# Kernel tuning notes

Measured on AMD Instinct MI355X. Metric: run time of the kernel, lower is better.

The kernel has to match this reference:

```python
import jax, jax.numpy as jnp
import numpy as np

LABEL_SIZE = 64
START = LABEL_SIZE - 2
STOP = LABEL_SIZE - 1
NEG = -10000.0


def setup_inputs() -> dict:
    key = jax.random.key(0)
    k1, k2 = jax.random.split(key)
    B, T, L = 512, 512, LABEL_SIZE
    emissions = jax.random.normal(k1, (B, T, L), dtype=jnp.float32)
    # xavier-uniform-ish init, then mask row START (nothing transitions INTO start
    # ... actually transitions[next, prev]: row START = transitions into START)
    bound = float(np.sqrt(6.0 / (L + L)))
    trans = jax.random.uniform(k2, (L, L), dtype=jnp.float32, minval=-bound, maxval=bound)
    trans = trans.at[START, :].set(NEG)   # never transition to START
    trans = trans.at[:, STOP].set(NEG)    # never transition from STOP
    return {"input": emissions, "transitions": trans}


def reference(input, transitions):
    # input: [B, T, L] emission scores; transitions[next_tag, prev_tag]: [L, L]
    B, T, L = input.shape
    init = jnp.full((B, L), NEG, dtype=input.dtype).at[:, START].set(0.0)

    def step(forward_var, emit_t):
        # forward_var: [B, L] (over prev tag); emit_t: [B, L] (over next tag)
        # scores[b, next, prev] = forward_var[b, prev] + transitions[next, prev]
        nv = jax.nn.logsumexp(forward_var[:, None, :] + transitions[None, :, :], axis=-1)
        return nv + emit_t, None

    forward_var, _ = jax.lax.scan(step, init, jnp.swapaxes(input, 0, 1))  # scan over T
    terminal = forward_var + transitions[STOP][None, :]
    return jax.nn.logsumexp(terminal, axis=-1)  # [B] log partition function
```

## Files before the change

### kernel.cpp

```cpp
#include <hip/hip_runtime.h>

#define NTAG 64
#define TLEN 512
#define START_TAG 62
#define STOP_TAG 63
#define NB 16

typedef __attribute__((ext_vector_type(4))) float    f32x4;
typedef __attribute__((ext_vector_type(8))) short    s16x8;
typedef __attribute__((ext_vector_type(2))) unsigned u32x2;
typedef __attribute__((ext_vector_type(4))) unsigned u32x4;

#if __has_builtin(__builtin_amdgcn_exp2f)
#define EXP2(x) __builtin_amdgcn_exp2f(x)
#else
#define EXP2(x) exp2f(x)
#endif

__device__ __forceinline__ unsigned cvtpk_bf16(float lo, float hi) {
    unsigned r;
    asm("v_cvt_pk_bf16_f32 %0, %1, %2" : "=v"(r) : "v"(lo), "v"(hi));
    return r;
}

__device__ __forceinline__ f32x4 mfma32(s16x8 a, s16x8 b, f32x4 c) {
    return __builtin_amdgcn_mfma_f32_16x16x32_bf16(a, b, c, 0, 0, 0);
}

__global__ __launch_bounds__(128) void crf_fwd_bwd(
    const float* __restrict__ emis,
    const float* __restrict__ trans,
    float* __restrict__ out)
{
    const int tile = blockIdx.x;
    const int tid  = threadIdx.x;
    const int lane = tid & 63;
    const int w    = tid >> 6;
    const int c    = lane & 15;
    const int g    = lane >> 4;
    const int b0   = tile * NB;

    const float L2E = 1.4426950408889634f;
    const float LN2 = 0.6931471805599453f;

    __shared__ float fy[64][17];
    __shared__ int   offb_sh[16];

    s16x8 Af[4][2];
    #pragma unroll
    for (int m = 0; m < 4; ++m) {
        #pragma unroll
        for (int kt = 0; kt < 2; ++kt) {
            float ev[8];
            #pragma unroll
            for (int jj = 0; jj < 8; ++jj) {
                const int r = 16 * m + c;
                const int k = 32 * kt + 16 * (jj >> 2) + 4 * g + (jj & 3);
                const float tv = (w == 0) ? trans[r * NTAG + k]
                                          : trans[k * NTAG + r];
                ev[jj] = EXP2(tv * L2E);
            }
            u32x4 p;
            p[0] = cvtpk_bf16(ev[0], ev[1]);
            p[1] = cvtpk_bf16(ev[2], ev[3]);
            p[2] = cvtpk_bf16(ev[4], ev[5]);
            p[3] = cvtpk_bf16(ev[6], ev[7]);
            Af[m][kt] = __builtin_bit_cast(s16x8, p);
        }
    }

    const float* ebase = emis + (size_t)(b0 + c) * (TLEN * NTAG);

    u32x2  Bf[4];
    f32x4  ym[4];
    f32x4  wq[4][4];
    int    off  = 0;
    int    eref = 0;

    #define PREF(slot, t) do {                                         \
        const float* _p = ebase + (t) * NTAG + 4 * g;                  \
        wq[slot][0] = *(const f32x4*)(_p +  0);                        \
        wq[slot][1] = *(const f32x4*)(_p + 16);                        \
        wq[slot][2] = *(const f32x4*)(_p + 32);                        \
        wq[slot][3] = *(const f32x4*)(_p + 48);                        \
    } while (0)

    #define BCAT(i) __builtin_bit_cast(s16x8,                          \
        (u32x4){Bf[2*(i)].x, Bf[2*(i)].y, Bf[2*(i)+1].x, Bf[2*(i)+1].y})

    #define MFMA_ALL() do {                                            \
        s16x8 B0 = BCAT(0), B1 = BCAT(1);                              \
        f32x4 a0 = {0.f,0.f,0.f,0.f}, a1 = a0, a2 = a0, a3 = a0;       \
        a0 = mfma32(Af[0][0], B0, a0);                                 \
        a1 = mfma32(Af[1][0], B0, a1);                                 \
        a2 = mfma32(Af[2][0], B0, a2);                                 \
        a3 = mfma32(Af[3][0], B0, a3);                                 \
        a0 = mfma32(Af[0][1], B1, a0);                                 \
        a1 = mfma32(Af[1][1], B1, a1);                                 \
        a2 = mfma32(Af[2][1], B1, a2);                                 \
        a3 = mfma32(Af[3][1], B1, a3);                                 \
        ym[0] = a0; ym[1] = a1; ym[2] = a2; ym[3] = a3;                \
    } while (0)

    #define COLMAX_UPDATE(mxv) do {                                    \
        float _m = (mxv);                                              \
        _m = fmaxf(_m, __shfl_xor(_m, 16, 64));                        \
        _m = fmaxf(_m, __shfl_xor(_m, 32, 64));                        \
        const int _ef = (int)((__float_as_uint(_m) >> 23) & 0xffu);    \
        eref = (_ef == 0 || _ef == 0xff) ? 0 : _ef - 127;              \
    } while (0)

    #define STEP_W(slot) do {                                          \
        const float fne = (float)(-eref);                              \
        off += eref;                                                   \
        MFMA_ALL();                                                    \
        float mx = 0.f;                                                \
        _Pragma("unroll")                                              \
        for (int m = 0; m < 4; ++m) {                                  \
            _Pragma("unroll")                                          \
            for (int j = 0; j < 4; ++j) {                              \
                ym[m][j] *= EXP2(fmaf(wq[slot][m][j], L2E, fne));      \
                mx = fmaxf(mx, ym[m][j]);                              \
            }                                                          \
            Bf[m].x = cvtpk_bf16(ym[m][0], ym[m][1]);                  \
            Bf[m].y = cvtpk_bf16(ym[m][2], ym[m][3]);                  \
        }                                                              \
        COLMAX_UPDATE(mx);                                             \
    } while (0)

    #define STEP_BARE() do {                                           \
        off += eref;                                                   \
        const float rs = __uint_as_float((unsigned)(127 - eref) << 23);\
        MFMA_ALL();                                                    \
        _Pragma("unroll")                                              \
        for (int m = 0; m < 4; ++m) ym[m] = ym[m] * rs;                \
    } while (0)

    if (w == 0) {
        Bf[0].x = 0u; Bf[0].y = 0u; Bf[1] = Bf[0]; Bf[2] = Bf[0];
        Bf[3].x = 0u; Bf[3].y = (g == 3) ? 0x3f80u : 0u;
        eref = 0;

        PREF(0, 0); PREF(1, 1); PREF(2, 2); PREF(3, 3);
        #pragma clang loop unroll(disable)
        for (int it = 0; it < 63; ++it) {
            const int t = it * 4;
            STEP_W(0); PREF(0, t + 4);
            STEP_W(1); PREF(1, t + 5);
            STEP_W(2); PREF(2, t + 6);
            STEP_W(3); PREF(3, t + 7);
        }
        STEP_W(0); STEP_W(1); STEP_W(2); STEP_W(3);
    } else {
        float smx = 0.f;
        #pragma unroll
        for (int m = 0; m < 4; ++m) {
            const float* _p = ebase + 511 * NTAG + 16 * m + 4 * g;
            f32x4 wv = *(const f32x4*)_p;
            float v[4];
            #pragma unroll
            for (int j = 0; j < 4; ++j) {
                const int r = 16 * m + 4 * g + j;
                v[j] = EXP2((trans[STOP_TAG * NTAG + r] + wv[j]) * L2E);
                smx = fmaxf(smx, v[j]);
            }
            Bf[m].x = cvtpk_bf16(v[0], v[1]);
            Bf[m].y = cvtpk_bf16(v[2], v[3]);
        }
        COLMAX_UPDATE(smx);

        PREF(0, 510); PREF(1, 509); PREF(2, 508); PREF(3, 507);
        #pragma clang loop unroll(disable)
        for (int it = 0; it < 63; ++it) {
            const int t = 510 - it * 4;
            STEP_W(0); PREF(0, t - 4);
            STEP_W(1); PREF(1, t - 5);
            STEP_W(2); PREF(2, t - 6);
            STEP_W(3); PREF(3, t - 7);
        }
        STEP_W(0); STEP_W(1); STEP_W(2);
        STEP_BARE();

        #pragma unroll
        for (int m = 0; m < 4; ++m)
            #pragma unroll
            for (int j = 0; j < 4; ++j)
                fy[lane][4 * m + j] = ym[m][j];
        if (lane < 16) offb_sh[lane] = off;
    }

    __syncthreads();

    if (w == 0) {
        float p = 0.f;
        #pragma unroll
        for (int m = 0; m < 4; ++m)
            #pragma unroll
            for (int j = 0; j < 4; ++j)
                p = fmaf(ym[m][j], fy[lane][4 * m + j], p);
        p += __shfl_xor(p, 16, 64);
        p += __shfl_xor(p, 32, 64);
        if (lane < 16)
            out[b0 + lane] = LN2 * (log2f(p) + (float)(off + offb_sh[lane]));
    }

    #undef PREF
    #undef BCAT
    #undef MFMA_ALL
    #undef COLMAX_UPDATE
    #undef STEP_W
    #undef STEP_BARE
}

extern "C" void kernel_launch(void* const* d_in, const int* in_sizes, int n_in,
                              void* d_out, int out_size, void* d_ws, size_t ws_size,
                              hipStream_t stream) {
    const float* emis  = (const float*)d_in[0];
    const float* trans = (const float*)d_in[1];
    float* out = (float*)d_out;
    (void)in_sizes; (void)n_in; (void)out_size; (void)d_ws; (void)ws_size;
    crf_fwd_bwd<<<512 / NB, 128, 0, stream>>>(emis, trans, out);
}
```

Measured before the change: 155.8 us.

## Overlap emission exp with MFMA and renormalize every other step with delayed scale

Restructures the serial forward/backward recurrence so the exponentials of the next step's emissions are computed while the current MFMAs are in flight, which takes the exp latency off the critical path. The per-step column-max rescale is now measured only on even steps and applied two steps later, so the reduction shuffles leave the dependency chain. The prefetch depth grows from 4 to 8 timesteps and the loop is unrolled by 8. The cost is more registers, and skipping renormalization on odd steps risks bf16/fp32 range growth between rescales.

```diff
diff --git a/kernel.cpp b/kernel.cpp
--- a/kernel.cpp
+++ b/kernel.cpp
@@ -69,94 +69,127 @@
         }
     }
 
-    const float* ebase = emis + (size_t)(b0 + c) * (TLEN * NTAG);
-
-    u32x2  Bf[4];
-    f32x4  ym[4];
-    f32x4  wq[4][4];
-    int    off  = 0;
-    int    eref = 0;
-
-    #define PREF(slot, t) do {                                         \
-        const float* _p = ebase + (t) * NTAG + 4 * g;                  \
+    const float* ebase = emis + (size_t)(b0 + c) * (TLEN * NTAG) + 4 * g;
+
+    f32x4 wq[8][4];
+    f32x4 peA[4], peB[4];
+    u32x2 Bf[4];
+    f32x4 ym[4];
+    int   off = 0;
+    int   erA = 0, erB = 0;
+
+    #define PREF_F(slot, t) do {                                       \
+        const float* _p = ebase + (t) * NTAG;                          \
         wq[slot][0] = *(const f32x4*)(_p +  0);                        \
         wq[slot][1] = *(const f32x4*)(_p + 16);                        \
         wq[slot][2] = *(const f32x4*)(_p + 32);                        \
         wq[slot][3] = *(const f32x4*)(_p + 48);                        \
     } while (0)
+    #define PREF_B(slot, tp) PREF_F(slot, 510 - (tp))
+
+    #define EXPQ(dst, slot) do {                                       \
+        _Pragma("unroll")                                              \
+        for (int m_ = 0; m_ < 4; ++m_) {                               \
+            dst[m_][0] = EXP2(wq[slot][m_][0] * L2E);                  \
+            dst[m_][1] = EXP2(wq[slot][m_][1] * L2E);                  \
+            dst[m_][2] = EXP2(wq[slot][m_][2] * L2E);                  \
+            dst[m_][3] = EXP2(wq[slot][m_][3] * L2E);                  \
+        }                                                              \
+    } while (0)
 
     #define BCAT(i) __builtin_bit_cast(s16x8,                          \
         (u32x4){Bf[2*(i)].x, Bf[2*(i)].y, Bf[2*(i)+1].x, Bf[2*(i)+1].y})
 
     #define MFMA_ALL() do {                                            \
-        s16x8 B0 = BCAT(0), B1 = BCAT(1);                              \
+        s16x8 B0_ = BCAT(0), B1_ = BCAT(1);                            \
         f32x4 a0 = {0.f,0.f,0.f,0.f}, a1 = a0, a2 = a0, a3 = a0;       \
-        a0 = mfma32(Af[0][0], B0, a0);                                 \
-        a1 = mfma32(Af[1][0], B0, a1);                                 \
-        a2 = mfma32(Af[2][0], B0, a2);                                 \
-        a3 = mfma32(Af[3][0], B0, a3);                                 \
-        a0 = mfma32(Af[0][1], B1, a0);                                 \
-        a1 = mfma32(Af[1][1], B1, a1);                                 \
-        a2 = mfma32(Af[2][1], B1, a2);                                 \
-        a3 = mfma32(Af[3][1], B1, a3);                                 \
+        a0 = mfma32(Af[0][0], B0_, a0); a1 = mfma32(Af[1][0], B0_, a1);\
+        a2 = mfma32(Af[2][0], B0_, a2); a3 = mfma32(Af[3][0], B0_, a3);\
+        a0 = mfma32(Af[0][1], B1_, a0); a1 = mfma32(Af[1][1], B1_, a1);\
+        a2 = mfma32(Af[2][1], B1_, a2); a3 = mfma32(Af[3][1], B1_, a3);\
         ym[0] = a0; ym[1] = a1; ym[2] = a2; ym[3] = a3;                \
     } while (0)
 
-    #define COLMAX_UPDATE(mxv) do {                                    \
+    #define PACK() do {                                                \
+        Bf[0].x = cvtpk_bf16(ym[0][0], ym[0][1]);                      \
+        Bf[0].y = cvtpk_bf16(ym[0][2], ym[0][3]);                      \
+        Bf[1].x = cvtpk_bf16(ym[1][0], ym[1][1]);                      \
+        Bf[1].y = cvtpk_bf16(ym[1][2], ym[1][3]);                      \
+        Bf[2].x = cvtpk_bf16(ym[2][0], ym[2][1]);                      \
+        Bf[2].y = cvtpk_bf16(ym[2][2], ym[2][3]);                      \
+        Bf[3].x = cvtpk_bf16(ym[3][0], ym[3][1]);                      \
+        Bf[3].y = cvtpk_bf16(ym[3][2], ym[3][3]);                      \
+    } while (0)
+
+    #define COLMAX_TO(dst, mxv) do {                                   \
         float _m = (mxv);                                              \
-        _m = fmaxf(_m, __shfl_xor(_m, 16, 64));                        \
-        _m = fmaxf(_m, __shfl_xor(_m, 32, 64));                        \
+        const float _s1 = __shfl_xor(_m, 16, 64);                      \
+        const float _s2 = __shfl_xor(_m, 32, 64);                      \
+        const float _s3 = __shfl_xor(_m, 48, 64);                      \
+        _m = fmaxf(fmaxf(_m, _s1), fmaxf(_s2, _s3));                   \
         const int _ef = (int)((__float_as_uint(_m) >> 23) & 0xffu);    \
-        eref = (_ef == 0 || _ef == 0xff) ? 0 : _ef - 127;              \
-    } while (0)
-
-    #define STEP_W(slot) do {                                          \
-        const float fne = (float)(-eref);                              \
-        off += eref;                                                   \
+        dst = (_ef == 0 || _ef == 0xff) ? 0 : _ef - 127;               \
+    } while (0)
+
+    #define CSTEP_E(u, PEC, PEN, ERAPP, ERMEAS, PRFM, tb) do {         \
+        off += ERAPP;                                                  \
+        const float rs_ =                                              \
+            __uint_as_float((unsigned)(127 - (ERAPP)) << 23);          \
         MFMA_ALL();                                                    \
-        float mx = 0.f;                                                \
-        _Pragma("unroll")                                              \
-        for (int m = 0; m < 4; ++m) {                                  \
-            _Pragma("unroll")                                          \
-            for (int j = 0; j < 4; ++j) {                              \
-                ym[m][j] *= EXP2(fmaf(wq[slot][m][j], L2E, fne));      \
-                mx = fmaxf(mx, ym[m][j]);                              \
-            }                                                          \
-            Bf[m].x = cvtpk_bf16(ym[m][0], ym[m][1]);                  \
-            Bf[m].y = cvtpk_bf16(ym[m][2], ym[m][3]);                  \
-        }                                                              \
-        COLMAX_UPDATE(mx);                                             \
-    } while (0)
-
-    #define STEP_BARE() do {                                           \
-        off += eref;                                                   \
-        const float rs = __uint_as_float((unsigned)(127 - eref) << 23);\
+        EXPQ(PEN, ((u) + 1) & 7);                                     \
+        ym[0] = ym[0] * PEC[0] * rs_; ym[1] = ym[1] * PEC[1] * rs_;    \
+        ym[2] = ym[2] * PEC[2] * rs_; ym[3] = ym[3] * PEC[3] * rs_;    \
+        PACK();                                                        \
+        float mx_ = fmaxf(fmaxf(fmaxf(ym[0][0], ym[0][1]),             \
+                                fmaxf(ym[0][2], ym[0][3])),            \
+                          fmaxf(fmaxf(ym[1][0], ym[1][1]),             \
+                                fmaxf(ym[1][2], ym[1][3])));           \
+        mx_ = fmaxf(mx_, fmaxf(fmaxf(ym[2][0], ym[2][1]),              \
+                               fmaxf(ym[2][2], ym[2][3])));            \
+        mx_ = fmaxf(mx_, fmaxf(fmaxf(ym[3][0], ym[3][1]),              \
+                               fmaxf(ym[3][2], ym[3][3])));            \
+        COLMAX_TO(ERMEAS, mx_);                                        \
+        PRFM((u), (tb) + (u) + 8);                                     \
+    } while (0)
+
+    #define CSTEP_O(u, PEC, PEN, PRFM, tb) do {                        \
         MFMA_ALL();                                                    \
-        _Pragma("unroll")                                              \
-        for (int m = 0; m < 4; ++m) ym[m] = ym[m] * rs;                \
-    } while (0)
+        EXPQ(PEN, ((u) + 1) & 7);                                     \
+        ym[0] *= PEC[0]; ym[1] *= PEC[1];                              \
+        ym[2] *= PEC[2]; ym[3] *= PEC[3];                              \
+        PACK();                                                        \
+        PRFM((u), (tb) + (u) + 8);                                     \
+    } while (0)
+
+    #define OCTET(PRFM, tb)                                            \
+        CSTEP_E(0, peA, peB, erB, erA, PRFM, tb);                      \
+        CSTEP_O(1, peB, peA, PRFM, tb);                                \
+        CSTEP_E(2, peA, peB, erA, erB, PRFM, tb);                      \
+        CSTEP_O(3, peB, peA, PRFM, tb);                                \
+        CSTEP_E(4, peA, peB, erB, erA, PRFM, tb);                      \
+        CSTEP_O(5, peB, peA, PRFM, tb);                                \
+        CSTEP_E(6, peA, peB, erA, erB, PRFM, tb);                      \
+        CSTEP_O(7, peB, peA, PRFM, tb);
 
     if (w == 0) {
         Bf[0].x = 0u; Bf[0].y = 0u; Bf[1] = Bf[0]; Bf[2] = Bf[0];
         Bf[3].x = 0u; Bf[3].y = (g == 3) ? 0x3f80u : 0u;
-        eref = 0;
-
-        PREF(0, 0); PREF(1, 1); PREF(2, 2); PREF(3, 3);
+        erA = 0; erB = 0;
+
+        PREF_F(0, 0); PREF_F(1, 1); PREF_F(2, 2); PREF_F(3, 3);
+        PREF_F(4, 4); PREF_F(5, 5); PREF_F(6, 6); PREF_F(7, 7);
+        EXPQ(peA, 0);
+
         #pragma clang loop unroll(disable)
-        for (int it = 0; it < 63; ++it) {
-            const int t = it * 4;
-            STEP_W(0); PREF(0, t + 4);
-            STEP_W(1); PREF(1, t + 5);
-            STEP_W(2); PREF(2, t + 6);
-            STEP_W(3); PREF(3, t + 7);
-        }
-        STEP_W(0); STEP_W(1); STEP_W(2); STEP_W(3);
+        for (int it = 0; it < 32; ++it) {
+            const int tb = it * 8;
+            OCTET(PREF_F, tb)
+        }
     } else {
         float smx = 0.f;
         #pragma unroll
         for (int m = 0; m < 4; ++m) {
-            const float* _p = ebase + 511 * NTAG + 16 * m + 4 * g;
-            f32x4 wv = *(const f32x4*)_p;
+            f32x4 wv = *(const f32x4*)(ebase + 511 * NTAG + 16 * m);
             float v[4];
             #pragma unroll
             for (int j = 0; j < 4; ++j) {
@@ -167,19 +200,32 @@
             Bf[m].x = cvtpk_bf16(v[0], v[1]);
             Bf[m].y = cvtpk_bf16(v[2], v[3]);
         }
-        COLMAX_UPDATE(smx);
-
-        PREF(0, 510); PREF(1, 509); PREF(2, 508); PREF(3, 507);
+        COLMAX_TO(erB, smx);
+        erA = 0;
+
+        PREF_B(0, 0); PREF_B(1, 1); PREF_B(2, 2); PREF_B(3, 3);
+        PREF_B(4, 4); PREF_B(5, 5); PREF_B(6, 6); PREF_B(7, 7);
+        EXPQ(peA, 0);
+
         #pragma clang loop unroll(disable)
-        for (int it = 0; it < 63; ++it) {
-            const int t = 510 - it * 4;
-            STEP_W(0); PREF(0, t - 4);
-            STEP_W(1); PREF(1, t - 5);
-            STEP_W(2); PREF(2, t - 6);
-            STEP_W(3); PREF(3, t - 7);
-        }
-        STEP_W(0); STEP_W(1); STEP_W(2);
-        STEP_BARE();
+        for (int it = 0; it < 31; ++it) {
+            const int tb = it * 8;
+            OCTET(PREF_B, tb)
+        }
+        {
+            const int tb = 248;
+            CSTEP_E(0, peA, peB, erB, erA, PREF_B, tb);
+            CSTEP_O(1, peB, peA, PREF_B, tb);
+            CSTEP_E(2, peA, peB, erA, erB, PREF_B, tb);
+            CSTEP_O(3, peB, peA, PREF_B, tb);
+            CSTEP_E(4, peA, peB, erB, erA, PREF_B, tb);
+            CSTEP_O(5, peB, peA, PREF_B, tb);
+            CSTEP_E(6, peA, peB, erA, erB, PREF_B, tb);
+        }
+        off += erB;
+        const float rs = __uint_as_float((unsigned)(127 - erB) << 23);
+        MFMA_ALL();
+        ym[0] *= rs; ym[1] *= rs; ym[2] *= rs; ym[3] *= rs;
 
         #pragma unroll
         for (int m = 0; m < 4; ++m)
@@ -204,12 +250,16 @@
             out[b0 + lane] = LN2 * (log2f(p) + (float)(off + offb_sh[lane]));
     }
 
-    #undef PREF
+    #undef PREF_F
+    #undef PREF_B
+    #undef EXPQ
     #undef BCAT
     #undef MFMA_ALL
-    #undef COLMAX_UPDATE
-    #undef STEP_W
-    #undef STEP_BARE
+    #undef PACK
+    #undef COLMAX_TO
+    #undef CSTEP_E
+    #undef CSTEP_O
+    #undef OCTET
 }
 
 extern "C" void kernel_launch(void* const* d_in, const int* in_sizes, int n_in,
```

Result: slower. 159.7 us (+2.5%).
